# Kernel optimization log

Measured on AMD Instinct MI355X. Metric: run time of the kernel, lower is better.

Reference implementation:

```python
import jax, jax.numpy as jnp
import numpy as np

EPS = 1e-3  # Keras BatchNormalization default epsilon
HEADS = 4
KEY_DEPTH = 16   # k
INTRA = 1        # u
VAL_DEPTH = 64   # v = kernel_out // heads = 256 // 4
C_IN = 256
B, HH, WW = 16, 32, 32
N = HH * WW      # == size of positional embedding


def setup_inputs() -> dict:
    key = jax.random.key(0)
    ks = jax.random.split(key, 6)
    x = jax.random.normal(ks[0], (B, HH, WW, C_IN), dtype=jnp.float32)
    # 1x1 conv kernels == dense matrices over the channel dim
    Wq = jax.random.normal(ks[1], (C_IN, KEY_DEPTH * HEADS), dtype=jnp.float32) * 0.05
    Wk = jax.random.normal(ks[2], (C_IN, KEY_DEPTH * INTRA), dtype=jnp.float32) * 0.05
    Wv = jax.random.normal(ks[3], (C_IN, VAL_DEPTH * INTRA), dtype=jnp.float32) * 0.05
    # BatchNorm (inference mode) parameters
    gamma_q = jnp.ones((KEY_DEPTH * HEADS,), jnp.float32)
    beta_q = jnp.zeros((KEY_DEPTH * HEADS,), jnp.float32)
    mean_q = jnp.zeros((KEY_DEPTH * HEADS,), jnp.float32)
    var_q = jnp.ones((KEY_DEPTH * HEADS,), jnp.float32)
    gamma_v = jnp.ones((VAL_DEPTH * INTRA,), jnp.float32)
    beta_v = jnp.zeros((VAL_DEPTH * INTRA,), jnp.float32)
    mean_v = jnp.zeros((VAL_DEPTH * INTRA,), jnp.float32)
    var_v = jnp.ones((VAL_DEPTH * INTRA,), jnp.float32)
    # Positional embedding: [size, size, key_depth, intra_depth], uniform init
    E = jax.random.uniform(ks[4], (N, N, KEY_DEPTH, INTRA), dtype=jnp.float32)
    return {
        'x': x, 'Wq': Wq, 'Wk': Wk, 'Wv': Wv,
        'gamma_q': gamma_q, 'beta_q': beta_q, 'mean_q': mean_q, 'var_q': var_q,
        'gamma_v': gamma_v, 'beta_v': beta_v, 'mean_v': mean_v, 'var_v': var_v,
        'E': E,
    }


def _bn(t, gamma, beta, mean, var):
    return gamma * (t - mean) / jnp.sqrt(var + EPS) + beta


def reference(x, Wq, Wk, Wv, gamma_q, beta_q, mean_q, var_q,
              gamma_v, beta_v, mean_v, var_v, E):
    b, hh, ww, _ = x.shape
    n = hh * ww
    # 1x1 conv projections (context c == x)
    q = jnp.einsum('bhwc,cd->bhwd', x, Wq)           # [b,hh,ww,h*k]
    k = jnp.einsum('bhwc,cd->bhwd', x, Wk)           # [b,hh,ww,u*k]
    v = jnp.einsum('bhwc,cd->bhwd', x, Wv)           # [b,hh,ww,u*v]
    q = _bn(q, gamma_q, beta_q, mean_q, var_q)
    v = _bn(v, gamma_v, beta_v, mean_v, var_v)
    # softmax over the channel axis (faithful to the source code)
    k = jax.nn.softmax(k, axis=-1)
    # rearranges: b hh ww (h k) -> b h k n ; b hh ww (u k) -> b u k n ; b hh ww (u v) -> b u v n
    q = q.reshape(b, n, HEADS, KEY_DEPTH).transpose(0, 2, 3, 1)   # [b,h,k,n]
    k = k.reshape(b, n, INTRA, KEY_DEPTH).transpose(0, 2, 3, 1)   # [b,u,k,n]
    v = v.reshape(b, n, INTRA, VAL_DEPTH).transpose(0, 2, 3, 1)   # [b,u,v,n]
    # content lambda: sum over intra-depth and positions
    lam_c = jnp.einsum('bukn,buvn->bkv', k, v)                    # [b,k,v]
    Yc = jnp.einsum('bhkn,bkv->bhvn', q, lam_c)                   # [b,h,v,n]
    # positional lambdas: E[n,m,k,u] contracted with v[b,u,v,m]
    lam_p = jnp.einsum('nmku,buvm->bnkv', E, v)                   # [b,n,k,v]
    Yp = jnp.einsum('bhkn,bnkv->bhvn', q, lam_p)                  # [b,h,v,n]
    Y = Yc + Yp                                                    # [b,h,v,n]
    # b h v n -> b hh ww (h v)
    out = Y.transpose(0, 3, 1, 2).reshape(b, hh, ww, HEADS * VAL_DEPTH)
    return out
```

## Files before the change

kernel.cpp:

```cpp
#include <hip/hip_runtime.h>
#include <stdint.h>

#define EPS 1e-3f

typedef __bf16 bf16x8 __attribute__((ext_vector_type(8)));
typedef float  f32x4  __attribute__((ext_vector_type(4)));

static __device__ __forceinline__ uint16_t f2bf(float f) {
  union { __bf16 b; uint16_t u; } r; r.b = (__bf16)f; return r.u;
}
static __device__ __forceinline__ uint32_t cvt2(float lo, float hi) {
  union { __bf16 b[2]; uint32_t u; } r;
  r.b[0] = (__bf16)lo; r.b[1] = (__bf16)hi;
  return r.u;
}
static __device__ __forceinline__ void gload_lds16(const void* g, void* l) {
  __builtin_amdgcn_global_load_lds(
      (const __attribute__((address_space(1))) unsigned int*)g,
      (__attribute__((address_space(3))) unsigned int*)l, 16, 0, 0);
}

__global__ __launch_bounds__(256) void wprep(
    const float* __restrict__ Wq, const float* __restrict__ Wk,
    const float* __restrict__ Wv, uint16_t* __restrict__ WtP)
{
  const int col = blockIdx.x, t = threadIdx.x;
  float val = (col < 64) ? Wq[t * 64 + col]
            : (col < 80) ? Wk[t * 16 + (col - 64)]
                         : Wv[t * 64 + (col - 80)];
  WtP[col * 264 + t] = f2bf(val);
}

__global__ __launch_bounds__(512) void proj_mfma(
    const float* __restrict__ x, const uint16_t* __restrict__ WtP,
    const float* __restrict__ gq, const float* __restrict__ bq,
    const float* __restrict__ mq, const float* __restrict__ vq,
    const float* __restrict__ gv, const float* __restrict__ bv,
    const float* __restrict__ mv, const float* __restrict__ vvp,
    float* __restrict__ Qf, uint16_t* __restrict__ VbfT,
    float* __restrict__ part)
{
  __shared__ __align__(16) char smem[143616];
  uint16_t* const xA = (uint16_t*)smem;
  char* const Wt = smem + 67584;

  const int t = threadIdx.x;
  const int wid = t >> 6, lane = t & 63;
  const int bid = blockIdx.x;
  const int b = bid >> 3, mc = bid & 7;
  const int r0 = b * 1024 + mc * 128;

#pragma unroll
  for (int i = 0; i < 10; ++i) {
    int off = (i * 512 + t) * 16;
    gload_lds16((const char*)WtP + off, Wt + off);
  }
  {
    const int row = t >> 2, ks0 = (t & 3) * 64;
    const float* src = x + (size_t)(r0 + row) * 256 + ks0;
    uint16_t* dstp = xA + row * 264 + ks0;
#pragma unroll
    for (int i = 0; i < 8; ++i) {
      float4 d0 = *(const float4*)(src + i * 8);
      float4 d1 = *(const float4*)(src + i * 8 + 4);
      uint4 q;
      q.x = cvt2(d0.x, d0.y); q.y = cvt2(d0.z, d0.w);
      q.z = cvt2(d1.x, d1.y); q.w = cvt2(d1.z, d1.w);
      *(uint4*)(dstp + i * 8) = q;
    }
  }
  __syncthreads();

  f32x4 acc[9];
#pragma unroll
  for (int f = 0; f < 9; ++f) acc[f] = f32x4{0.f, 0.f, 0.f, 0.f};
  const int arow = wid * 16 + (lane & 15);
#pragma unroll
  for (int kst = 0; kst < 8; ++kst) {
    const int sb = kst * 64 + ((lane >> 4) << 4);
    bf16x8 af = *(const bf16x8*)((const char*)xA + arow * 528 + sb);
#pragma unroll
    for (int f = 0; f < 9; ++f) {
      const int crow = f * 16 + (lane & 15);
      bf16x8 bfr = *(const bf16x8*)(Wt + crow * 528 + sb);
      acc[f] = __builtin_amdgcn_mfma_f32_16x16x32_bf16(af, bfr, acc[f], 0, 0, 0);
    }
  }

  const int cl = lane & 15;
  const int rbase = wid * 16 + ((lane >> 4) << 2);

  float qs[4], qb[4], qm[4], vs[4], vb[4], vm[4];
#pragma unroll
  for (int f = 0; f < 4; ++f) {
    const int c = f * 16 + cl;
    qs[f] = gq[c] * rsqrtf(vq[c] + EPS); qb[f] = bq[c]; qm[f] = mq[c];
    vs[f] = gv[c] * rsqrtf(vvp[c] + EPS); vb[f] = bv[c]; vm[f] = mv[c];
  }
#pragma unroll
  for (int f = 0; f < 4; ++f)
#pragma unroll
    for (int r = 0; r < 4; ++r)
      Qf[(size_t)(r0 + rbase + r) * 64 + f * 16 + cl] =
          (acc[f][r] - qm[f]) * qs[f] + qb[f];
  float ex[4];
#pragma unroll
  for (int r = 0; r < 4; ++r) {
    float kv = acc[4][r];
    float mx = kv;
#pragma unroll
    for (int d = 1; d < 16; d <<= 1) mx = fmaxf(mx, __shfl_xor(mx, d, 64));
    float e = __expf(kv - mx);
    float sm = e;
#pragma unroll
    for (int d = 1; d < 16; d <<= 1) sm += __shfl_xor(sm, d, 64);
    ex[r] = e / sm;
  }
  float vv[4][4];
#pragma unroll
  for (int f = 0; f < 4; ++f)
#pragma unroll
    for (int r = 0; r < 4; ++r)
      vv[f][r] = (acc[5 + f][r] - vm[f]) * vs[f] + vb[f];

  __syncthreads();
  float* const vt = (float*)smem;
  float* const ks = (float*)(smem + 128 * 65 * 4);
#pragma unroll
  for (int r = 0; r < 4; ++r) ks[(rbase + r) * 20 + cl] = ex[r];
#pragma unroll
  for (int f = 0; f < 4; ++f)
#pragma unroll
    for (int r = 0; r < 4; ++r) vt[(rbase + r) * 65 + f * 16 + cl] = vv[f][r];
  __syncthreads();

  {
    const int v = t & 63, grp = t >> 6;
#pragma unroll
    for (int h = 0; h < 2; ++h) {
      uint4 q;
      q.x = cvt2(vt[(grp * 16 + h * 8 + 0) * 65 + v], vt[(grp * 16 + h * 8 + 1) * 65 + v]);
      q.y = cvt2(vt[(grp * 16 + h * 8 + 2) * 65 + v], vt[(grp * 16 + h * 8 + 3) * 65 + v]);
      q.z = cvt2(vt[(grp * 16 + h * 8 + 4) * 65 + v], vt[(grp * 16 + h * 8 + 5) * 65 + v]);
      q.w = cvt2(vt[(grp * 16 + h * 8 + 6) * 65 + v], vt[(grp * 16 + h * 8 + 7) * 65 + v]);
      *(uint4*)&VbfT[(size_t)(b * 64 + v) * 1024 + mc * 128 + grp * 16 + h * 8] = q;
    }
  }
  {
    const int kq = (t >> 6) & 3, half = t >> 8, v = t & 63;
    const int mbase = half * 64;
    float a0 = 0.f, a1 = 0.f, a2 = 0.f, a3 = 0.f;
#pragma unroll 4
    for (int m = 0; m < 64; ++m) {
      float vvx = vt[(mbase + m) * 65 + v];
      a0 = fmaf(ks[(mbase + m) * 20 + kq * 4 + 0], vvx, a0);
      a1 = fmaf(ks[(mbase + m) * 20 + kq * 4 + 1], vvx, a1);
      a2 = fmaf(ks[(mbase + m) * 20 + kq * 4 + 2], vvx, a2);
      a3 = fmaf(ks[(mbase + m) * 20 + kq * 4 + 3], vvx, a3);
    }
    float* dst = part + ((size_t)(b * 16 + mc * 2 + half) << 10) + (kq * 4) * 64 + v;
    dst[0] = a0; dst[64] = a1; dst[128] = a2; dst[192] = a3;
  }
}

__global__ __launch_bounds__(256) void lamc_reduce(const float* __restrict__ part,
                                                   float* __restrict__ Lc)
{
  const int gid = blockIdx.x * 256 + threadIdx.x;
  const int b = gid >> 10, r = gid & 1023;
  const float* p = part + ((size_t)b << 14) + r;
  float s = 0.f;
#pragma unroll
  for (int mc = 0; mc < 16; ++mc) s += p[mc << 10];
  Lc[((size_t)b << 10) + r] = s;
}

__global__ __launch_bounds__(512, 2) void gemm_out(
    const float* __restrict__ E,
    const uint16_t* __restrict__ VbfT,
    const float* __restrict__ Qf,
    const float* __restrict__ Lc,
    float* __restrict__ out)
{
  __shared__ __align__(16) char smem[131072];
  char* const A0 = smem;
  char* const B0 = smem + 32768;
  char* const A1 = smem + 65536;
  char* const B1 = smem + 98304;

  const int t = threadIdx.x;
  const int wid = t >> 6, lane = t & 63;
  const int wm = wid >> 2, wn = wid & 3;
  const int bid = blockIdx.x;
  const int xcd = bid & 7, idx = bid >> 3;
  const int rb = xcd * 8 + (idx >> 2);
  const int cb = idx & 3;
  const int col0 = cb * 256;
  const int n0 = rb * 16;

  const int kq = t & 3;
  const int mp = (t >> 2) & 31;
  const int nb = t >> 7;
  const float* Eb = E + ((size_t)n0 << 14);

  int awoff[4][4];
#pragma unroll
  for (int it = 0; it < 4; ++it)
#pragma unroll
    for (int j = 0; j < 4; ++j) {
      int row = (it * 4 + nb) * 16 + kq * 4 + j;
      awoff[it][j] = row * 128 + ((mp * 4) ^ ((row & 7) << 4));
    }

  const uint16_t* bptr[4];
  int bdst[4];
  {
    const uint16_t* Bb = VbfT + ((size_t)col0 << 10);
#pragma unroll
    for (int it = 0; it < 4; ++it) {
      int id = it * 512 + t;
      int row = id >> 3, seg = id & 7;
      bptr[it] = Bb + (row << 10) + ((seg ^ (row & 7)) << 3);
      bdst[it] = id * 16;
    }
  }

  f32x4 acc[8][4];
#pragma unroll
  for (int i = 0; i < 8; ++i)
#pragma unroll
    for (int j = 0; j < 4; ++j) acc[i][j] = f32x4{0.f, 0.f, 0.f, 0.f};

  float4 ra[4], rbx[4];

#pragma unroll
  for (int it = 0; it < 4; ++it) {
    size_t base = ((size_t)(it * 4 + nb) << 14) + ((size_t)(mp * 2) << 4) + (kq << 2);
    ra[it]  = *(const float4*)(Eb + base);
    rbx[it] = *(const float4*)(Eb + base + 16);
  }
#pragma unroll
  for (int it = 0; it < 4; ++it) gload_lds16(bptr[it], B0 + bdst[it]);
#pragma unroll
  for (int it = 0; it < 4; ++it) {
    const float* da = (const float*)&ra[it];
    const float* db = (const float*)&rbx[it];
#pragma unroll
    for (int j = 0; j < 4; ++j)
      *(uint32_t*)(A0 + awoff[it][j]) = cvt2(da[j], db[j]);
  }
  __syncthreads();

#pragma unroll 1
  for (int kt = 0; kt < 16; ++kt) {
    char* Ac = (kt & 1) ? A1 : A0;
    char* Bc = (kt & 1) ? B1 : B0;
    char* An = (kt & 1) ? A0 : A1;
    char* Bn = (kt & 1) ? B0 : B1;
    if (kt < 15) {
      const int m0n = (kt + 1) * 64;
#pragma unroll
      for (int it = 0; it < 4; ++it) {
        size_t base = ((size_t)(it * 4 + nb) << 14) +
                      ((size_t)(m0n + mp * 2) << 4) + (kq << 2);
        ra[it]  = *(const float4*)(Eb + base);
        rbx[it] = *(const float4*)(Eb + base + 16);
      }
#pragma unroll
      for (int it = 0; it < 4; ++it) gload_lds16(bptr[it] + m0n, Bn + bdst[it]);
    }
    __builtin_amdgcn_s_setprio(1);
#pragma unroll
    for (int kk = 0; kk < 2; ++kk) {
      bf16x8 a[8], b[4];
      const int s = kk * 4 + (lane >> 4);
#pragma unroll
      for (int i = 0; i < 8; ++i) {
        int row = wm * 128 + i * 16 + (lane & 15);
        a[i] = *(const bf16x8*)(Ac + row * 128 + ((s ^ (row & 7)) << 4));
      }
#pragma unroll
      for (int j = 0; j < 4; ++j) {
        int row = wn * 64 + j * 16 + (lane & 15);
        b[j] = *(const bf16x8*)(Bc + row * 128 + ((s ^ (row & 7)) << 4));
      }
#pragma unroll
      for (int i = 0; i < 8; ++i)
#pragma unroll
        for (int j = 0; j < 4; ++j)
          acc[i][j] = __builtin_amdgcn_mfma_f32_16x16x32_bf16(a[i], b[j], acc[i][j], 0, 0, 0);
    }
    __builtin_amdgcn_s_setprio(0);
    if (kt < 15) {
#pragma unroll
      for (int it = 0; it < 4; ++it) {
        const float* da = (const float*)&ra[it];
        const float* db = (const float*)&rbx[it];
#pragma unroll
        for (int j = 0; j < 4; ++j)
          *(uint32_t*)(An + awoff[it][j]) = cvt2(da[j], db[j]);
      }
    }
    __syncthreads();
  }

  float* Cs = (float*)smem;
  const int b0 = cb * 4;
#pragma unroll
  for (int p = 0; p < 4; ++p) {
    if (wm == (p >> 1)) {
#pragma unroll
      for (int il = 0; il < 4; ++il) {
        const int i = ((p & 1) << 2) + il;
#pragma unroll
        for (int j = 0; j < 4; ++j) {
          const int col = wn * 64 + j * 16 + (lane & 15);
          const int bb = b0 + (col >> 6), v = col & 63;
#pragma unroll
          for (int r = 0; r < 4; ++r) {
            const int rl = il * 16 + ((lane >> 4) << 2) + r;
            const int k = rl & 15;
            Cs[rl * 258 + col] = acc[i][j][r] + Lc[(size_t)(((bb << 4) + k) << 6) + v];
          }
        }
      }
    }
    __syncthreads();
    {
      const int v = t & 63;
#pragma unroll
      for (int c = 0; c < 8; ++c) {
        const int combo = (wid << 3) + c;
        const int n_l = combo >> 4;
        const int b_l = (combo >> 2) & 3;
        const int h = combo & 3;
        const int n = n0 + (p << 2) + n_l;
        const int bb = b0 + b_l;
        const float* qp = Qf + (((size_t)(bb << 10) + n) << 6) + (h << 4);
        float sum = 0.f;
#pragma unroll
        for (int k = 0; k < 16; ++k)
          sum = fmaf(qp[k], Cs[((n_l << 4) + k) * 258 + (b_l << 6) + v], sum);
        out[(((size_t)(bb << 10) + n) << 8) + (h << 6) + v] = sum;
      }
    }
    __syncthreads();
  }
}

extern "C" void kernel_launch(void* const* d_in, const int* in_sizes, int n_in,
                              void* d_out, int out_size, void* d_ws, size_t ws_size,
                              hipStream_t stream) {
  const float* x   = (const float*)d_in[0];
  const float* Wq  = (const float*)d_in[1];
  const float* Wk  = (const float*)d_in[2];
  const float* Wv  = (const float*)d_in[3];
  const float* gq  = (const float*)d_in[4];
  const float* bq  = (const float*)d_in[5];
  const float* mq  = (const float*)d_in[6];
  const float* vq  = (const float*)d_in[7];
  const float* gv  = (const float*)d_in[8];
  const float* bv  = (const float*)d_in[9];
  const float* mv  = (const float*)d_in[10];
  const float* vvp = (const float*)d_in[11];
  const float* E   = (const float*)d_in[12];
  float* out = (float*)d_out;

  char* ws = (char*)d_ws;
  uint16_t* VbfT = (uint16_t*)(ws);
  float*    Qf   = (float*)(ws + (size_t)(2 << 20));
  float*    part = (float*)(ws + (size_t)(6 << 20));
  float*    Lc   = (float*)(ws + (size_t)(7 << 20));
  uint16_t* WtP  = (uint16_t*)(ws + (size_t)(7 << 20) + 65536);

  hipLaunchKernelGGL(wprep, dim3(144), dim3(256), 0, stream, Wq, Wk, Wv, WtP);
  hipLaunchKernelGGL(proj_mfma, dim3(128), dim3(512), 0, stream, x, WtP,
                     gq, bq, mq, vq, gv, bv, mv, vvp, Qf, VbfT, part);
  hipLaunchKernelGGL(lamc_reduce, dim3(64), dim3(256), 0, stream, part, Lc);
  hipLaunchKernelGGL(gemm_out, dim3(256), dim3(512), 0, stream, E, VbfT, Qf, Lc, out);
}
```

Baseline: 77.58 us.

## Reassociate positional lambda: contract E with Q first, then with V

The final kernel now contracts E with the query per position (producing a per-position [m,b*h] tile via MFMA) and then multiplies by V, instead of first forming lam_p = E·V for all n and then contracting with Q. Q is stored as bf16 rather than fp32, and the content-lambda term is computed directly from Lc in shared memory. This changes the tiling to 4 positions per block, with E streamed in double-buffered chunks and an intermediate bf16 rounding of the E·Q product. It risks extra precision loss and lower occupancy (launch bounds 1 block).

Measured after the change: 131.6 us. +69.7%, slower.

```diff
diff --git a/kernel.cpp b/kernel.cpp
--- a/kernel.cpp
+++ b/kernel.cpp
@@ -13,6 +13,9 @@
   union { __bf16 b[2]; uint32_t u; } r;
   r.b[0] = (__bf16)lo; r.b[1] = (__bf16)hi;
   return r.u;
+}
+static __device__ __forceinline__ float bf2f(uint16_t u) {
+  union { uint32_t u; float f; } c; c.u = ((uint32_t)u) << 16; return c.f;
 }
 static __device__ __forceinline__ void gload_lds16(const void* g, void* l) {
   __builtin_amdgcn_global_load_lds(
@@ -37,7 +40,7 @@
     const float* __restrict__ mq, const float* __restrict__ vq,
     const float* __restrict__ gv, const float* __restrict__ bv,
     const float* __restrict__ mv, const float* __restrict__ vvp,
-    float* __restrict__ Qf, uint16_t* __restrict__ VbfT,
+    uint16_t* __restrict__ Qb, uint16_t* __restrict__ VbfT,
     float* __restrict__ part)
 {
   __shared__ __align__(16) char smem[143616];
@@ -63,10 +66,10 @@
     for (int i = 0; i < 8; ++i) {
       float4 d0 = *(const float4*)(src + i * 8);
       float4 d1 = *(const float4*)(src + i * 8 + 4);
-      uint4 q;
-      q.x = cvt2(d0.x, d0.y); q.y = cvt2(d0.z, d0.w);
-      q.z = cvt2(d1.x, d1.y); q.w = cvt2(d1.z, d1.w);
-      *(uint4*)(dstp + i * 8) = q;
+      uint4 qv;
+      qv.x = cvt2(d0.x, d0.y); qv.y = cvt2(d0.z, d0.w);
+      qv.z = cvt2(d1.x, d1.y); qv.w = cvt2(d1.z, d1.w);
+      *(uint4*)(dstp + i * 8) = qv;
     }
   }
   __syncthreads();
@@ -90,19 +93,19 @@
   const int cl = lane & 15;
   const int rbase = wid * 16 + ((lane >> 4) << 2);
 
-  float qs[4], qb[4], qm[4], vs[4], vb[4], vm[4];
+  float qs[4], qbb[4], qm[4], vs[4], vb[4], vm[4];
 #pragma unroll
   for (int f = 0; f < 4; ++f) {
     const int c = f * 16 + cl;
-    qs[f] = gq[c] * rsqrtf(vq[c] + EPS); qb[f] = bq[c]; qm[f] = mq[c];
+    qs[f] = gq[c] * rsqrtf(vq[c] + EPS); qbb[f] = bq[c]; qm[f] = mq[c];
     vs[f] = gv[c] * rsqrtf(vvp[c] + EPS); vb[f] = bv[c]; vm[f] = mv[c];
   }
 #pragma unroll
   for (int f = 0; f < 4; ++f)
 #pragma unroll
     for (int r = 0; r < 4; ++r)
-      Qf[(size_t)(r0 + rbase + r) * 64 + f * 16 + cl] =
-          (acc[f][r] - qm[f]) * qs[f] + qb[f];
+      Qb[(size_t)(r0 + rbase + r) * 64 + f * 16 + cl] =
+          f2bf((acc[f][r] - qm[f]) * qs[f] + qbb[f]);
   float ex[4];
 #pragma unroll
   for (int r = 0; r < 4; ++r) {
@@ -137,13 +140,13 @@
   {
     const int v = t & 63, grp = t >> 6;
 #pragma unroll
-    for (int h = 0; h < 2; ++h) {
-      uint4 q;
-      q.x = cvt2(vt[(grp * 16 + h * 8 + 0) * 65 + v], vt[(grp * 16 + h * 8 + 1) * 65 + v]);
-      q.y = cvt2(vt[(grp * 16 + h * 8 + 2) * 65 + v], vt[(grp * 16 + h * 8 + 3) * 65 + v]);
-      q.z = cvt2(vt[(grp * 16 + h * 8 + 4) * 65 + v], vt[(grp * 16 + h * 8 + 5) * 65 + v]);
-      q.w = cvt2(vt[(grp * 16 + h * 8 + 6) * 65 + v], vt[(grp * 16 + h * 8 + 7) * 65 + v]);
-      *(uint4*)&VbfT[(size_t)(b * 64 + v) * 1024 + mc * 128 + grp * 16 + h * 8] = q;
+    for (int hh = 0; hh < 2; ++hh) {
+      uint4 qv;
+      qv.x = cvt2(vt[(grp * 16 + hh * 8 + 0) * 65 + v], vt[(grp * 16 + hh * 8 + 1) * 65 + v]);
+      qv.y = cvt2(vt[(grp * 16 + hh * 8 + 2) * 65 + v], vt[(grp * 16 + hh * 8 + 3) * 65 + v]);
+      qv.z = cvt2(vt[(grp * 16 + hh * 8 + 4) * 65 + v], vt[(grp * 16 + hh * 8 + 5) * 65 + v]);
+      qv.w = cvt2(vt[(grp * 16 + hh * 8 + 6) * 65 + v], vt[(grp * 16 + hh * 8 + 7) * 65 + v]);
+      *(uint4*)&VbfT[(size_t)(b * 64 + v) * 1024 + mc * 128 + grp * 16 + hh * 8] = qv;
     }
   }
   {
@@ -175,176 +178,153 @@
   Lc[((size_t)b << 10) + r] = s;
 }
 
-__global__ __launch_bounds__(512, 2) void gemm_out(
+__global__ __launch_bounds__(512, 1) void lambda_out(
     const float* __restrict__ E,
     const uint16_t* __restrict__ VbfT,
-    const float* __restrict__ Qf,
+    const uint16_t* __restrict__ Qb,
     const float* __restrict__ Lc,
     float* __restrict__ out)
 {
-  __shared__ __align__(16) char smem[131072];
-  char* const A0 = smem;
-  char* const B0 = smem + 32768;
-  char* const A1 = smem + 65536;
-  char* const B1 = smem + 98304;
-
+  __shared__ __align__(16) char smem[98304];
   const int t = threadIdx.x;
   const int wid = t >> 6, lane = t & 63;
-  const int wm = wid >> 2, wn = wid & 3;
-  const int bid = blockIdx.x;
-  const int xcd = bid & 7, idx = bid >> 3;
-  const int rb = xcd * 8 + (idx >> 2);
-  const int cb = idx & 3;
-  const int col0 = cb * 256;
-  const int n0 = rb * 16;
-
-  const int kq = t & 3;
-  const int mp = (t >> 2) & 31;
-  const int nb = t >> 7;
-  const float* Eb = E + ((size_t)n0 << 14);
-
-  int awoff[4][4];
-#pragma unroll
-  for (int it = 0; it < 4; ++it)
-#pragma unroll
-    for (int j = 0; j < 4; ++j) {
-      int row = (it * 4 + nb) * 16 + kq * 4 + j;
-      awoff[it][j] = row * 128 + ((mp * 4) ^ ((row & 7) << 4));
-    }
-
-  const uint16_t* bptr[4];
-  int bdst[4];
-  {
-    const uint16_t* Bb = VbfT + ((size_t)col0 << 10);
-#pragma unroll
-    for (int it = 0; it < 4; ++it) {
-      int id = it * 512 + t;
-      int row = id >> 3, seg = id & 7;
-      bptr[it] = Bb + (row << 10) + ((seg ^ (row & 7)) << 3);
-      bdst[it] = id * 16;
-    }
-  }
-
-  f32x4 acc[8][4];
-#pragma unroll
-  for (int i = 0; i < 8; ++i)
-#pragma unroll
-    for (int j = 0; j < 4; ++j) acc[i][j] = f32x4{0.f, 0.f, 0.f, 0.f};
-
-  float4 ra[4], rbx[4];
-
-#pragma unroll
-  for (int it = 0; it < 4; ++it) {
-    size_t base = ((size_t)(it * 4 + nb) << 14) + ((size_t)(mp * 2) << 4) + (kq << 2);
-    ra[it]  = *(const float4*)(Eb + base);
-    rbx[it] = *(const float4*)(Eb + base + 16);
-  }
-#pragma unroll
-  for (int it = 0; it < 4; ++it) gload_lds16(bptr[it], B0 + bdst[it]);
-#pragma unroll
-  for (int it = 0; it < 4; ++it) {
-    const float* da = (const float*)&ra[it];
-    const float* db = (const float*)&rbx[it];
-#pragma unroll
-    for (int j = 0; j < 4; ++j)
-      *(uint32_t*)(A0 + awoff[it][j]) = cvt2(da[j], db[j]);
-  }
-  __syncthreads();
+  const int l = lane & 15, q = lane >> 4;
+  const int n0 = blockIdx.x * 4;
+  const int h = l >> 2, nl = l & 3;
+
+  f32x4 acc[2][4];
+#pragma unroll
+  for (int bl = 0; bl < 2; ++bl)
+#pragma unroll
+    for (int vf = 0; vf < 4; ++vf) acc[bl][vf] = f32x4{0.f, 0.f, 0.f, 0.f};
+
+#pragma unroll
+  for (int i = 0; i < 8; ++i) {
+    int off = (i * 512 + t) * 16;
+    gload_lds16((const char*)Lc + off, smem + 20480 + off);
+  }
+  if (t < 256) {
+    const int n = t >> 6, bh = t & 63, b = bh >> 2, hh = bh & 3;
+    const uint4* src = (const uint4*)(Qb + ((size_t)((b << 10) + n0 + n) << 6) + (hh << 4));
+    char* dst = smem + n * 5120 + bh * 80;
+    uint4 z = {0, 0, 0, 0};
+    uint4 q0 = src[0], q1 = src[1];
+    *(uint4*)(dst) = q0; *(uint4*)(dst + 16) = q1;
+    *(uint4*)(dst + 32) = z; *(uint4*)(dst + 48) = z;
+  }
+  __syncthreads();
+
+  {
+    const float* LcF = (const float*)(smem + 20480);
+#pragma unroll
+    for (int bl = 0; bl < 2; ++bl) {
+      const int b = wid * 2 + bl;
+      float qv[16];
+#pragma unroll
+      for (int kk = 0; kk < 16; ++kk)
+        qv[kk] = bf2f(*(const uint16_t*)(smem + nl * 5120 + (b * 4 + h) * 80 + kk * 2));
+#pragma unroll
+      for (int vf = 0; vf < 4; ++vf) {
+#pragma unroll
+        for (int kk = 0; kk < 16; ++kk) {
+          const float4 lc = *(const float4*)(LcF + b * 1024 + kk * 64 + vf * 16 + q * 4);
+          acc[bl][vf][0] = fmaf(qv[kk], lc.x, acc[bl][vf][0]);
+          acc[bl][vf][1] = fmaf(qv[kk], lc.y, acc[bl][vf][1]);
+          acc[bl][vf][2] = fmaf(qv[kk], lc.z, acc[bl][vf][2]);
+          acc[bl][vf][3] = fmaf(qv[kk], lc.w, acc[bl][vf][3]);
+        }
+      }
+    }
+  }
+  __syncthreads();
+
+  {
+    uint4 z = {0, 0, 0, 0};
+    const int buf = t >> 8, rest = t & 255;
+    char* dz = smem + 20480 + buf * 20480 + (rest >> 6) * 5120 + (rest & 63) * 80 + 32;
+    *(uint4*)(dz) = z; *(uint4*)(dz + 16) = z;
+  }
+  const int spair = t >> 1, skh = t & 1;
+  const int sn = spair >> 6, sm = spair & 63;
+  const float* Esrc = E + ((size_t)(n0 + sn) << 14) + ((size_t)sm << 4) + skh * 8;
+  {
+    float4 f0 = *(const float4*)Esrc, f1 = *(const float4*)(Esrc + 4);
+    uint4 w; w.x = cvt2(f0.x, f0.y); w.y = cvt2(f0.z, f0.w);
+    w.z = cvt2(f1.x, f1.y); w.w = cvt2(f1.z, f1.w);
+    *(uint4*)(smem + 20480 + sn * 5120 + sm * 80 + skh * 16) = w;
+  }
+  __syncthreads();
+
+  const int n_tp = wid >> 1, cf0 = (wid & 1) * 2;
+  const int p0 = cf0 * 64 + (l >> 2) * 16 + (l & 3) * 4 + n_tp;
+  const int p1 = p0 + 64;
+
+  float4 f0a, f0b;
 
 #pragma unroll 1
-  for (int kt = 0; kt < 16; ++kt) {
-    char* Ac = (kt & 1) ? A1 : A0;
-    char* Bc = (kt & 1) ? B1 : B0;
-    char* An = (kt & 1) ? A0 : A1;
-    char* Bn = (kt & 1) ? B0 : B1;
-    if (kt < 15) {
-      const int m0n = (kt + 1) * 64;
-#pragma unroll
-      for (int it = 0; it < 4; ++it) {
-        size_t base = ((size_t)(it * 4 + nb) << 14) +
-                      ((size_t)(m0n + mp * 2) << 4) + (kq << 2);
-        ra[it]  = *(const float4*)(Eb + base);
-        rbx[it] = *(const float4*)(Eb + base + 16);
+  for (int mc = 0; mc < 16; ++mc) {
+    const int cur = mc & 1;
+    char* EmC = smem + 20480 + cur * 20480;
+    char* EmN = smem + 20480 + (cur ^ 1) * 20480;
+    if (mc < 15) {
+      const float* s = Esrc + ((size_t)(mc + 1) << 10);
+      f0a = *(const float4*)s; f0b = *(const float4*)(s + 4);
+    }
+    {
+      bf16x8 bq0 = *(const bf16x8*)(smem + n_tp * 5120 + (cf0 * 16 + l) * 80 + q * 16);
+      bf16x8 bq1 = *(const bf16x8*)(smem + n_tp * 5120 + ((cf0 + 1) * 16 + l) * 80 + q * 16);
+#pragma unroll
+      for (int mf = 0; mf < 4; ++mf) {
+        bf16x8 ae = *(const bf16x8*)(EmC + n_tp * 5120 + (mf * 16 + l) * 80 + q * 16);
+        f32x4 t0 = __builtin_amdgcn_mfma_f32_16x16x32_bf16(ae, bq0, f32x4{0.f,0.f,0.f,0.f}, 0, 0, 0);
+        f32x4 t1 = __builtin_amdgcn_mfma_f32_16x16x32_bf16(ae, bq1, f32x4{0.f,0.f,0.f,0.f}, 0, 0, 0);
+        const int c = 2 * mf + (q >> 1);
+        uint2 w0; w0.x = cvt2(t0[0], t0[1]); w0.y = cvt2(t0[2], t0[3]);
+        uint2 w1; w1.x = cvt2(t1[0], t1[1]); w1.y = cvt2(t1[2], t1[3]);
+        *(uint2*)(smem + 61440 + p0 * 144 + (((c) ^ (p0 & 7)) << 4) + ((q & 1) << 3)) = w0;
+        *(uint2*)(smem + 61440 + p1 * 144 + (((c) ^ (p1 & 7)) << 4) + ((q & 1) << 3)) = w1;
       }
-#pragma unroll
-      for (int it = 0; it < 4; ++it) gload_lds16(bptr[it] + m0n, Bn + bdst[it]);
-    }
-    __builtin_amdgcn_s_setprio(1);
-#pragma unroll
-    for (int kk = 0; kk < 2; ++kk) {
-      bf16x8 a[8], b[4];
-      const int s = kk * 4 + (lane >> 4);
-#pragma unroll
-      for (int i = 0; i < 8; ++i) {
-        int row = wm * 128 + i * 16 + (lane & 15);
-        a[i] = *(const bf16x8*)(Ac + row * 128 + ((s ^ (row & 7)) << 4));
-      }
-#pragma unroll
-      for (int j = 0; j < 4; ++j) {
-        int row = wn * 64 + j * 16 + (lane & 15);
-        b[j] = *(const bf16x8*)(Bc + row * 128 + ((s ^ (row & 7)) << 4));
-      }
-#pragma unroll
-      for (int i = 0; i < 8; ++i)
-#pragma unroll
-        for (int j = 0; j < 4; ++j)
-          acc[i][j] = __builtin_amdgcn_mfma_f32_16x16x32_bf16(a[i], b[j], acc[i][j], 0, 0, 0);
-    }
-    __builtin_amdgcn_s_setprio(0);
-    if (kt < 15) {
-#pragma unroll
-      for (int it = 0; it < 4; ++it) {
-        const float* da = (const float*)&ra[it];
-        const float* db = (const float*)&rbx[it];
-#pragma unroll
-        for (int j = 0; j < 4; ++j)
-          *(uint32_t*)(An + awoff[it][j]) = cvt2(da[j], db[j]);
-      }
     }
     __syncthreads();
-  }
-
-  float* Cs = (float*)smem;
-  const int b0 = cb * 4;
-#pragma unroll
-  for (int p = 0; p < 4; ++p) {
-    if (wm == (p >> 1)) {
-#pragma unroll
-      for (int il = 0; il < 4; ++il) {
-        const int i = ((p & 1) << 2) + il;
-#pragma unroll
-        for (int j = 0; j < 4; ++j) {
-          const int col = wn * 64 + j * 16 + (lane & 15);
-          const int bb = b0 + (col >> 6), v = col & 63;
-#pragma unroll
-          for (int r = 0; r < 4; ++r) {
-            const int rl = il * 16 + ((lane >> 4) << 2) + r;
-            const int k = rl & 15;
-            Cs[rl * 258 + col] = acc[i][j][r] + Lc[(size_t)(((bb << 4) + k) << 6) + v];
+    {
+      const size_t m0 = (size_t)mc * 64;
+#pragma unroll
+      for (int bl = 0; bl < 2; ++bl) {
+        const int b = wid * 2 + bl;
+        const char* trow = smem + 61440 + (b * 16 + l) * 144;
+        const int px = (b * 16 + l) & 7;
+#pragma unroll
+        for (int kst = 0; kst < 2; ++kst) {
+          bf16x8 bT = *(const bf16x8*)(trow + (((kst * 4 + q) ^ px) << 4));
+#pragma unroll
+          for (int vf = 0; vf < 4; ++vf) {
+            const uint16_t* vs = VbfT + (((size_t)(b * 64 + vf * 16 + l)) << 10)
+                                 + m0 + kst * 32 + q * 8;
+            bf16x8 aV = *(const bf16x8*)vs;
+            acc[bl][vf] = __builtin_amdgcn_mfma_f32_16x16x32_bf16(aV, bT, acc[bl][vf], 0, 0, 0);
           }
         }
       }
+      if (mc < 15) {
+        uint4 w; w.x = cvt2(f0a.x, f0a.y); w.y = cvt2(f0a.z, f0a.w);
+        w.z = cvt2(f0b.x, f0b.y); w.w = cvt2(f0b.z, f0b.w);
+        *(uint4*)(EmN + sn * 5120 + sm * 80 + skh * 16) = w;
+      }
     }
     __syncthreads();
-    {
-      const int v = t & 63;
-#pragma unroll
-      for (int c = 0; c < 8; ++c) {
-        const int combo = (wid << 3) + c;
-        const int n_l = combo >> 4;
-        const int b_l = (combo >> 2) & 3;
-        const int h = combo & 3;
-        const int n = n0 + (p << 2) + n_l;
-        const int bb = b0 + b_l;
-        const float* qp = Qf + (((size_t)(bb << 10) + n) << 6) + (h << 4);
-        float sum = 0.f;
-#pragma unroll
-        for (int k = 0; k < 16; ++k)
-          sum = fmaf(qp[k], Cs[((n_l << 4) + k) * 258 + (b_l << 6) + v], sum);
-        out[(((size_t)(bb << 10) + n) << 8) + (h << 6) + v] = sum;
-      }
-    }
-    __syncthreads();
+  }
+
+#pragma unroll
+  for (int bl = 0; bl < 2; ++bl) {
+    const int b = wid * 2 + bl;
+#pragma unroll
+    for (int vf = 0; vf < 4; ++vf) {
+      float4 o;
+      o.x = acc[bl][vf][0]; o.y = acc[bl][vf][1];
+      o.z = acc[bl][vf][2]; o.w = acc[bl][vf][3];
+      *(float4*)(out + (((size_t)((b << 10) + n0 + nl)) << 8)
+                 + (h << 6) + vf * 16 + q * 4) = o;
+    }
   }
 }
 
@@ -368,14 +348,14 @@
 
   char* ws = (char*)d_ws;
   uint16_t* VbfT = (uint16_t*)(ws);
-  float*    Qf   = (float*)(ws + (size_t)(2 << 20));
-  float*    part = (float*)(ws + (size_t)(6 << 20));
-  float*    Lc   = (float*)(ws + (size_t)(7 << 20));
-  uint16_t* WtP  = (uint16_t*)(ws + (size_t)(7 << 20) + 65536);
+  uint16_t* Qb   = (uint16_t*)(ws + (size_t)(2 << 20));
+  float*    part = (float*)(ws + (size_t)(4 << 20));
+  float*    Lc   = (float*)(ws + (size_t)(5 << 20));
+  uint16_t* WtP  = (uint16_t*)(ws + (size_t)(5 << 20) + 65536);
 
   hipLaunchKernelGGL(wprep, dim3(144), dim3(256), 0, stream, Wq, Wk, Wv, WtP);
   hipLaunchKernelGGL(proj_mfma, dim3(128), dim3(512), 0, stream, x, WtP,
-                     gq, bq, mq, vq, gv, bv, mv, vvp, Qf, VbfT, part);
+                     gq, bq, mq, vq, gv, bv, mv, vvp, Qb, VbfT, part);
   hipLaunchKernelGGL(lamc_reduce, dim3(64), dim3(256), 0, stream, part, Lc);
-  hipLaunchKernelGGL(gemm_out, dim3(256), dim3(512), 0, stream, E, VbfT, Qf, Lc, out);
-}
+  hipLaunchKernelGGL(lambda_out, dim3(256), dim3(512), 0, stream, E, VbfT, Qb, Lc, out);
+}
```
